# Kernel optimization log

Hardware: AMD Instinct MI355X
Metric: run time of the kernel (lower is better)

The kernel has to match this reference:

```python
import jax, jax.numpy as jnp
import numpy as np

S = 1.0   # scale s
M = 0.4   # margin m
EPS = 1e-12  # F.normalize eps


def _l2norm_rows(a):
    # F.normalize(a, dim=1): row-wise L2 normalization
    n = jnp.linalg.norm(a, axis=1, keepdims=True)
    return a / jnp.maximum(n, EPS)


def _half_loss(sim):
    # unique-label branch: positive is the diagonal, all off-diagonal are negatives
    N = sim.shape[0]
    num = S * (jnp.diagonal(sim) - M)                       # [N]
    offdiag = jnp.exp(S * sim) * (1.0 - jnp.eye(N, dtype=sim.dtype))
    denom = jnp.exp(num) + jnp.sum(offdiag, axis=1)         # [N]
    return num - jnp.log(denom)


def setup_inputs() -> dict:
    key = jax.random.key(0)
    k1, k2 = jax.random.split(key)
    N, D = 8192, 256
    return {
        "x1": jax.random.normal(k1, (N, D), dtype=jnp.float32),
        "x2": jax.random.normal(k2, (N, D), dtype=jnp.float32),
        "sentence_id": jnp.arange(N, dtype=jnp.int32),  # unique labels -> more_label=False branch
    }


def reference(x1, x2, sentence_id):
    # x12[i,j] row-normalized similarity of x1_i against all x2_j (and symmetric)
    x12 = _l2norm_rows(x1 @ x2.T)   # [N, N]
    x21 = _l2norm_rows(x2 @ x1.T)   # [N, N]
    L12 = _half_loss(x12)
    L21 = _half_loss(x21)
    loss = -jnp.mean(L12) - jnp.mean(L21)
    return loss, L12, L21
```

## Files before the change

### kernel.cpp

```cpp
#include <hip/hip_runtime.h>
#include <cstdint>
#include <cstddef>


#define NROWS 8192
#define DIMK 256
#define MARGIN 0.4f
#define LOG2E 1.4426950408889634f
#define LN2 0.6931471805599453f

typedef short short8 __attribute__((ext_vector_type(8)));
typedef float f32x4 __attribute__((ext_vector_type(4)));

__device__ __forceinline__ unsigned short f2bf(float f) {
  union { float f; unsigned u; } v; v.f = f;
  unsigned r = (v.u + 0x7fffu + ((v.u >> 16) & 1u)) >> 16;
  return (unsigned short)r;
}

__device__ __forceinline__ unsigned char f2fp8(float f) {
  union { float f; unsigned u; } v; v.f = f;
  const unsigned s = (v.u >> 24) & 0x80u;
  const unsigned au = v.u & 0x7fffffffu;
  if (au >= 0x43e00000u) return (unsigned char)(s | 0x7eu);
  int e = (int)(au >> 23) - 127;
  if (e >= -6) {
    unsigned mfull = (au & 0x7fffffu) | 0x800000u;
    unsigned r = (mfull + 0x7ffffu + ((mfull >> 20) & 1u)) >> 20;
    if (r == 16u) { r = 8u; ++e; }
    return (unsigned char)(s | ((unsigned)(e + 7) << 3) | (r & 7u));
  }
  float scaled = __builtin_fabsf(f) * 512.0f;
  unsigned n = (unsigned)(scaled + 0.5f);
  if (n >= 8u) return (unsigned char)(s | 0x08u);
  return (unsigned char)(s | n);
}

__device__ __forceinline__ void gl_lds16(const void* g, void* l) {
  __builtin_amdgcn_global_load_lds((const __attribute__((address_space(1))) void*)g,
                                   (__attribute__((address_space(3))) void*)l, 16, 0, 0);
}

__device__ __forceinline__ float fexp(float x) {
  return __builtin_amdgcn_exp2f(x * LOG2E);
}

__global__ __launch_bounds__(256)
void k_prep(const float* __restrict__ x1, const float* __restrict__ x2,
            unsigned short* __restrict__ Ab, unsigned short* __restrict__ Bb,
            unsigned char* __restrict__ A8, unsigned char* __restrict__ B8,
            float* __restrict__ diag, float* __restrict__ zero_region) {
  const int t = threadIdx.x;
  if (blockIdx.x < 2048) {
    const int row = blockIdx.x * 4 + (t >> 6);
    const int l = t & 63;
    const float4 a = ((const float4*)(x1 + (size_t)row * DIMK))[l];
    const float4 b = ((const float4*)(x2 + (size_t)row * DIMK))[l];
    ushort4 ua, ub;
    ua.x = f2bf(a.x); ua.y = f2bf(a.y); ua.z = f2bf(a.z); ua.w = f2bf(a.w);
    ub.x = f2bf(b.x); ub.y = f2bf(b.y); ub.z = f2bf(b.z); ub.w = f2bf(b.w);
    ((ushort4*)(Ab + (size_t)row * DIMK))[l] = ua;
    ((ushort4*)(Bb + (size_t)row * DIMK))[l] = ub;
    uchar4 qa, qb;
    qa.x = f2fp8(a.x); qa.y = f2fp8(a.y); qa.z = f2fp8(a.z); qa.w = f2fp8(a.w);
    qb.x = f2fp8(b.x); qb.y = f2fp8(b.y); qb.z = f2fp8(b.z); qb.w = f2fp8(b.w);
    ((uchar4*)(A8 + (size_t)row * DIMK))[l] = qa;
    ((uchar4*)(B8 + (size_t)row * DIMK))[l] = qb;
    float d = a.x * b.x + a.y * b.y + a.z * b.z + a.w * b.w;
#pragma unroll
    for (int m = 1; m < 64; m <<= 1) d += __shfl_xor(d, m);
    if (l == 0) diag[row] = d;
  } else {
    const size_t off = (size_t)(blockIdx.x - 2048) * 1024 + t * 4;
    float4 z = {0.f, 0.f, 0.f, 0.f};
    *(float4*)(zero_region + off) = z;
  }
}

__global__ __launch_bounds__(256)
void k_syrk(const unsigned short* __restrict__ Ab, const unsigned short* __restrict__ Bb,
            float* __restrict__ M1, float* __restrict__ M2) {
  __shared__ unsigned short As[64 * 32];
  __shared__ unsigned short Bs[64 * 32];
  const int t = threadIdx.x, w = t >> 6, l = t & 63, quad = l >> 4, l15 = l & 15;
  const int mat = blockIdx.z & 1;
  const int kseg = blockIdx.z >> 1;
  const unsigned short* X = mat ? Bb : Ab;
  float* Mo = mat ? M2 : M1;
  const int a0 = blockIdx.y * 64, b0 = blockIdx.x * 64;
  const int wr = (w >> 1) * 32, wc = (w & 1) * 32;
  f32x4 acc[2][2] = {};
  const int nn = t & 31, cb = t >> 5;
  const int c0 = cb * 8;
  const int nb = kseg * 512;
  for (int n0 = nb; n0 < nb + 512; n0 += 32) {
    short8 va = *(const short8*)(X + (size_t)(n0 + nn) * DIMK + a0 + c0);
    short8 vb = *(const short8*)(X + (size_t)(n0 + nn) * DIMK + b0 + c0);
#pragma unroll
    for (int i = 0; i < 8; ++i) {
      const int c = c0 + i;
      const int sl = (((nn >> 3) ^ ((c >> 1) & 3)) << 3) + (nn & 7);
      As[c * 32 + sl] = va[i];
      Bs[c * 32 + sl] = vb[i];
    }
    __syncthreads();
    short8 af[2], bg[2];
#pragma unroll
    for (int i = 0; i < 2; ++i) {
      const int ra = wr + i * 16 + l15;
      af[i] = *(const short8*)&As[ra * 32 + ((quad ^ ((ra >> 1) & 3)) << 3)];
      const int rb = wc + i * 16 + l15;
      bg[i] = *(const short8*)&Bs[rb * 32 + ((quad ^ ((rb >> 1) & 3)) << 3)];
    }
#pragma unroll
    for (int i = 0; i < 2; ++i)
#pragma unroll
      for (int j = 0; j < 2; ++j)
        acc[i][j] = __builtin_amdgcn_mfma_f32_16x16x32_bf16(af[i], bg[j], acc[i][j], 0, 0, 0);
    __syncthreads();
  }
#pragma unroll
  for (int i = 0; i < 2; ++i)
#pragma unroll
    for (int j = 0; j < 2; ++j)
#pragma unroll
      for (int r = 0; r < 4; ++r) {
        const int lr = wr + i * 16 + quad * 4 + r;
        const int lc = wc + j * 16 + l15;
        atomicAdd(&Mo[(size_t)(a0 + lr) * 256 + b0 + lc], acc[i][j][r]);
      }
}

__global__ __launch_bounds__(256)
void k_gemmN(const unsigned short* __restrict__ Ab, const unsigned short* __restrict__ Bb,
             const float* __restrict__ M1, const float* __restrict__ M2,
             const float* __restrict__ x1, const float* __restrict__ x2,
             float* __restrict__ rowsq, float* __restrict__ colsq) {
  __shared__ unsigned short As[2][4096];
  __shared__ unsigned short Bs[2][4096];
  const int t = threadIdx.x, w = t >> 6, l = t & 63, quad = l >> 4, l15 = l & 15;
  const unsigned short* A;
  const float* Mf;
  const float* Xf;
  float* sq;
  if (blockIdx.z == 0) { A = Ab; Mf = M2; Xf = x1; sq = rowsq; }
  else                 { A = Bb; Mf = M1; Xf = x2; sq = colsq; }
  const int row0 = blockIdx.x * 128;
  const int col0 = blockIdx.y * 128;
  const int wr = (w >> 1) * 64, wc = (w & 1) * 64;
  f32x4 acc[4][4] = {};

  const int sr0 = l >> 2, slot = l & 3;
  const int cA = w * 2, cB = w * 2 + 1;
  const int rA = cA * 16 + sr0, rB = cB * 16 + sr0;
  const int scA = (slot ^ ((rA >> 1) & 3)) << 3;
  const int scB = (slot ^ ((rB >> 1) & 3)) << 3;
  const unsigned short* pA0 = A + (size_t)(row0 + rA) * DIMK + scA;
  const unsigned short* pA1 = A + (size_t)(row0 + rB) * DIMK + scB;
  const int dA0 = cA * 512 + l * 8, dA1 = cB * 512 + l * 8;

  auto stageB = [&](int k0, int buf) {
#pragma unroll
    for (int g = 0; g < 2; ++g) {
      const int e = g * 2048 + t * 8;
      const int c = e >> 5, kk = e & 31;
      const float4 v0 = *(const float4*)(Mf + (size_t)(col0 + c) * 256 + k0 + kk);
      const float4 v1 = *(const float4*)(Mf + (size_t)(col0 + c) * 256 + k0 + kk + 4);
      ushort4 u0, u1;
      u0.x = f2bf(v0.x); u0.y = f2bf(v0.y); u0.z = f2bf(v0.z); u0.w = f2bf(v0.w);
      u1.x = f2bf(v1.x); u1.y = f2bf(v1.y); u1.z = f2bf(v1.z); u1.w = f2bf(v1.w);
      const int sw = ((kk >> 3) ^ ((c >> 1) & 3)) << 3;
      *(ushort4*)&Bs[buf][c * 32 + sw] = u0;
      *(ushort4*)&Bs[buf][c * 32 + sw + 4] = u1;
    }
  };
  auto issueA = [&](int k0, int buf) {
    gl_lds16(pA0 + k0, &As[buf][dA0]);
    gl_lds16(pA1 + k0, &As[buf][dA1]);
  };

  stageB(0, 0);
  issueA(0, 0);
#pragma unroll
  for (int k = 0; k < 8; ++k) {
    const int cur = k & 1;
    __syncthreads();
    if (k < 7) { stageB((k + 1) * 32, cur ^ 1); issueA((k + 1) * 32, cur ^ 1); }
    short8 af[4], bg[4];
#pragma unroll
    for (int i = 0; i < 4; ++i) {
      const int ra = wr + i * 16 + l15;
      af[i] = *(const short8*)&As[cur][ra * 32 + ((quad ^ ((ra >> 1) & 3)) << 3)];
      const int rb = wc + i * 16 + l15;
      bg[i] = *(const short8*)&Bs[cur][rb * 32 + ((quad ^ ((rb >> 1) & 3)) << 3)];
    }
#pragma unroll
    for (int i = 0; i < 4; ++i)
#pragma unroll
      for (int j = 0; j < 4; ++j)
        acc[i][j] = __builtin_amdgcn_mfma_f32_16x16x32_bf16(af[i], bg[j], acc[i][j], 0, 0, 0);
  }

#pragma unroll
  for (int i = 0; i < 4; ++i) {
#pragma unroll
    for (int r = 0; r < 4; ++r) {
      const int lr = wr + i * 16 + quad * 4 + r;
      const float* xr = Xf + (size_t)(row0 + lr) * DIMK + col0 + wc;
      float rp = 0.f;
#pragma unroll
      for (int j = 0; j < 4; ++j) rp += acc[i][j][r] * xr[j * 16 + l15];
      rp += __shfl_xor(rp, 1); rp += __shfl_xor(rp, 2);
      rp += __shfl_xor(rp, 4); rp += __shfl_xor(rp, 8);
      if (l15 == 0) atomicAdd(&sq[row0 + lr], rp);
    }
  }
}

__global__ __launch_bounds__(256)
void k_gemmE(const unsigned char* __restrict__ A8, const unsigned char* __restrict__ B8,
             const float* __restrict__ rowsq, const float* __restrict__ colsq,
             float* __restrict__ rowExp, float* __restrict__ colExp) {
  __shared__ unsigned char As[2][8192];
  __shared__ unsigned char Bs[2][8192];
  __shared__ float cRow[128];
  __shared__ float cCol[128];

  const int t = threadIdx.x;
  const int w = t >> 6;
  const int l = t & 63;
  const int quad = l >> 4;
  const int l15 = l & 15;
  const int row0 = blockIdx.x * 128;
  const int col0 = blockIdx.y * 128;
  const int wr = (w >> 1) * 64;
  const int wc = (w & 1) * 64;

  if (t < 128) cRow[t] = LOG2E * rsqrtf(rowsq[row0 + t]);
  else cCol[t - 128] = LOG2E * rsqrtf(colsq[col0 + t - 128]);

  f32x4 acc[4][4] = {};

  const int srow = t >> 1;
  const int shalf = (t & 1) * 16;
  const unsigned char* gA = A8 + (size_t)(row0 + srow) * DIMK + shalf;
  const unsigned char* gB = B8 + (size_t)(col0 + srow) * DIMK + shalf;
  const int d0 = t * 16, d1 = 4096 + t * 16;

  auto issue = [&](int k0, int buf) {
    gl_lds16(gA + k0, &As[buf][d0]);
    gl_lds16(gA + k0 + 32, &As[buf][d1]);
    gl_lds16(gB + k0, &Bs[buf][d0]);
    gl_lds16(gB + k0 + 32, &Bs[buf][d1]);
  };

  issue(0, 0);
#pragma unroll
  for (int it = 0; it < 4; ++it) {
    const int cur = it & 1;
    __syncthreads();
    if (it < 3) issue((it + 1) * 64, cur ^ 1);
#pragma unroll
    for (int kc = 0; kc < 2; ++kc) {
      long a_[4], b_[4];
#pragma unroll
      for (int i = 0; i < 4; ++i) {
        const int ra = wr + i * 16 + l15;
        a_[i] = *(const long*)&As[cur][kc * 4096 + ra * 32 + quad * 8];
        const int rb = wc + i * 16 + l15;
        b_[i] = *(const long*)&Bs[cur][kc * 4096 + rb * 32 + quad * 8];
      }
#pragma unroll
      for (int i = 0; i < 4; ++i)
#pragma unroll
        for (int j = 0; j < 4; ++j)
          acc[i][j] = __builtin_amdgcn_mfma_f32_16x16x32_fp8_fp8(a_[i], b_[j], acc[i][j], 0, 0, 0);
    }
  }

  float cj[4];
#pragma unroll
  for (int j = 0; j < 4; ++j) cj[j] = cCol[wc + j * 16 + l15];
  float colpart[4] = {0.f, 0.f, 0.f, 0.f};
#pragma unroll
  for (int i = 0; i < 4; ++i) {
#pragma unroll
    for (int r = 0; r < 4; ++r) {
      const int lr = wr + i * 16 + quad * 4 + r;
      const float ci = cRow[lr];
      float rp = 0.f;
#pragma unroll
      for (int j = 0; j < 4; ++j) {
        const float g = acc[i][j][r];
        rp += __builtin_amdgcn_exp2f(g * ci);
        colpart[j] += __builtin_amdgcn_exp2f(g * cj[j]);
      }
      rp += __shfl_xor(rp, 1); rp += __shfl_xor(rp, 2);
      rp += __shfl_xor(rp, 4); rp += __shfl_xor(rp, 8);
      if (l15 == 0) atomicAdd(&rowExp[row0 + lr], rp);
    }
  }
#pragma unroll
  for (int j = 0; j < 4; ++j) {
    float cp = colpart[j];
    cp += __shfl_xor(cp, 16); cp += __shfl_xor(cp, 32);
    if (l < 16) atomicAdd(&colExp[col0 + wc + j * 16 + l15], cp);
  }
}

__global__ __launch_bounds__(1024)
void k_final(const float* __restrict__ rowsq, const float* __restrict__ colsq,
             const float* __restrict__ diag, const float* __restrict__ rowExp,
             const float* __restrict__ colExp, float* __restrict__ out,
             double* __restrict__ lossAcc, int* __restrict__ doneCnt) {
  const int t = threadIdx.x;
  const int i = blockIdx.x * 1024 + t;
  const float d = diag[i];
  const float s1 = d * rsqrtf(rowsq[i]);
  const float s2 = d * rsqrtf(colsq[i]);
  const float n1 = s1 - MARGIN, n2 = s2 - MARGIN;
  const float L1 = n1 - LN2 * __builtin_amdgcn_logf(rowExp[i] - fexp(s1) + fexp(n1));
  const float L2 = n2 - LN2 * __builtin_amdgcn_logf(colExp[i] - fexp(s2) + fexp(n2));
  out[1 + i] = L1;
  out[1 + NROWS + i] = L2;
  double part = (double)L1 + (double)L2;
#pragma unroll
  for (int m = 1; m < 64; m <<= 1) part += __shfl_xor(part, m);
  __shared__ double red[16];
  if ((t & 63) == 0) red[t >> 6] = part;
  __syncthreads();
  if (t == 0) {
    double s = 0.0;
#pragma unroll
    for (int q = 0; q < 16; ++q) s += red[q];
    atomicAdd(lossAcc, s);
    __threadfence();
    if (atomicAdd(doneCnt, 1) == 7) {
      const double la =
          __hip_atomic_load(lossAcc, __ATOMIC_ACQUIRE, __HIP_MEMORY_SCOPE_AGENT);
      out[0] = (float)(-la / (double)NROWS);
    }
  }
}

extern "C" void kernel_launch(void* const* d_in, const int* in_sizes, int n_in,
                              void* d_out, int out_size, void* d_ws, size_t ws_size,
                              hipStream_t stream) {
  const float* x1 = (const float*)d_in[0];
  const float* x2 = (const float*)d_in[1];
  float* out = (float*)d_out;
  char* ws = (char*)d_ws;

  unsigned short* Ab = (unsigned short*)(ws);
  unsigned short* Bb = (unsigned short*)(ws + 4194304);
  float* M1 = (float*)(ws + 8388608);
  float* M2 = (float*)(ws + 8650752);
  float* rowsq = (float*)(ws + 8912896);
  float* colsq = (float*)(ws + 8945664);
  float* rowExp = (float*)(ws + 8978432);
  float* colExp = (float*)(ws + 9011200);
  char* ctrl = ws + 9043968;
  double* lossAcc = (double*)(ctrl);
  int* doneCnt = (int*)(ctrl + 256);
  float* diag = (float*)(ws + 9048064);
  unsigned char* A8 = (unsigned char*)(ws + 9080832);
  unsigned char* B8 = (unsigned char*)(ws + 11177984);

  k_prep<<<2209, 256, 0, stream>>>(x1, x2, Ab, Bb, A8, B8, diag,
                                   (float*)(ws + 8388608));
  k_syrk<<<dim3(4, 4, 32), 256, 0, stream>>>(Ab, Bb, M1, M2);
  k_gemmN<<<dim3(64, 2, 2), 256, 0, stream>>>(Ab, Bb, M1, M2, x1, x2, rowsq, colsq);
  k_gemmE<<<dim3(64, 64), 256, 0, stream>>>(A8, B8, rowsq, colsq, rowExp, colExp);
  k_final<<<8, 1024, 0, stream>>>(rowsq, colsq, diag, rowExp, colExp, out,
                                  lossAcc, doneCnt);
}
```

Measured before the change: 188.7 us.

## Double-buffer syrk staging and stream fp32 Gram tiles directly into LDS

k_syrk now double-buffers its LDS tiles, with one barrier per step, and writes packed 32-bit pairs instead of scalar shorts. Each block covers twice the K range, so the launch halves the split-K count and the number of atomic adds. k_gemmN stops converting the M matrices to bf16 in registers before storing to LDS. It loads fp32 directly with async global-to-LDS copies and converts to bf16 when building fragments, at the cost of double the LDS footprint and simpler rounding.

Result: slower. 197.8 us (+4.8%).

```diff
diff --git a/kernel.cpp b/kernel.cpp
--- a/kernel.cpp
+++ b/kernel.cpp
@@ -80,8 +80,8 @@
 __global__ __launch_bounds__(256)
 void k_syrk(const unsigned short* __restrict__ Ab, const unsigned short* __restrict__ Bb,
             float* __restrict__ M1, float* __restrict__ M2) {
-  __shared__ unsigned short As[64 * 32];
-  __shared__ unsigned short Bs[64 * 32];
+  __shared__ unsigned short As[2][2048];
+  __shared__ unsigned short Bs[2][2048];
   const int t = threadIdx.x, w = t >> 6, l = t & 63, quad = l >> 4, l15 = l & 15;
   const int mat = blockIdx.z & 1;
   const int kseg = blockIdx.z >> 1;
@@ -90,34 +90,48 @@
   const int a0 = blockIdx.y * 64, b0 = blockIdx.x * 64;
   const int wr = (w >> 1) * 32, wc = (w & 1) * 32;
   f32x4 acc[2][2] = {};
-  const int nn = t & 31, cb = t >> 5;
-  const int c0 = cb * 8;
-  const int nb = kseg * 512;
-  for (int n0 = nb; n0 < nb + 512; n0 += 32) {
-    short8 va = *(const short8*)(X + (size_t)(n0 + nn) * DIMK + a0 + c0);
-    short8 vb = *(const short8*)(X + (size_t)(n0 + nn) * DIMK + b0 + c0);
-#pragma unroll
-    for (int i = 0; i < 8; ++i) {
+  const int n2 = t & 15, c0 = (t >> 4) * 4;
+  const int nb = kseg * 1024;
+
+  auto stage = [&](int n0, int buf) {
+    const unsigned short* r0 = X + (size_t)(n0 + 2 * n2) * DIMK;
+    const unsigned short* r1 = X + (size_t)(n0 + 2 * n2 + 1) * DIMK;
+    const ushort4 a0v = *(const ushort4*)(r0 + a0 + c0);
+    const ushort4 a1v = *(const ushort4*)(r1 + a0 + c0);
+    const ushort4 b0v = *(const ushort4*)(r0 + b0 + c0);
+    const ushort4 b1v = *(const ushort4*)(r1 + b0 + c0);
+    const unsigned short pa0[4] = {a0v.x, a0v.y, a0v.z, a0v.w};
+    const unsigned short pa1[4] = {a1v.x, a1v.y, a1v.z, a1v.w};
+    const unsigned short pb0[4] = {b0v.x, b0v.y, b0v.z, b0v.w};
+    const unsigned short pb1[4] = {b1v.x, b1v.y, b1v.z, b1v.w};
+#pragma unroll
+    for (int i = 0; i < 4; ++i) {
       const int c = c0 + i;
-      const int sl = (((nn >> 3) ^ ((c >> 1) & 3)) << 3) + (nn & 7);
-      As[c * 32 + sl] = va[i];
-      Bs[c * 32 + sl] = vb[i];
-    }
+      const int ss = (n2 >> 2) ^ ((c >> 1) & 3);
+      const int pos = c * 32 + ss * 8 + ((2 * n2) & 7);
+      *(unsigned*)&As[buf][pos] = (unsigned)pa0[i] | ((unsigned)pa1[i] << 16);
+      *(unsigned*)&Bs[buf][pos] = (unsigned)pb0[i] | ((unsigned)pb1[i] << 16);
+    }
+  };
+
+  stage(nb, 0);
+  for (int it = 0; it < 32; ++it) {
+    const int cur = it & 1;
     __syncthreads();
+    if (it < 31) stage(nb + (it + 1) * 32, cur ^ 1);
     short8 af[2], bg[2];
 #pragma unroll
     for (int i = 0; i < 2; ++i) {
       const int ra = wr + i * 16 + l15;
-      af[i] = *(const short8*)&As[ra * 32 + ((quad ^ ((ra >> 1) & 3)) << 3)];
+      af[i] = *(const short8*)&As[cur][ra * 32 + ((quad ^ ((ra >> 1) & 3)) << 3)];
       const int rb = wc + i * 16 + l15;
-      bg[i] = *(const short8*)&Bs[rb * 32 + ((quad ^ ((rb >> 1) & 3)) << 3)];
+      bg[i] = *(const short8*)&Bs[cur][rb * 32 + ((quad ^ ((rb >> 1) & 3)) << 3)];
     }
 #pragma unroll
     for (int i = 0; i < 2; ++i)
 #pragma unroll
       for (int j = 0; j < 2; ++j)
         acc[i][j] = __builtin_amdgcn_mfma_f32_16x16x32_bf16(af[i], bg[j], acc[i][j], 0, 0, 0);
-    __syncthreads();
   }
 #pragma unroll
   for (int i = 0; i < 2; ++i)
@@ -137,7 +151,7 @@
              const float* __restrict__ x1, const float* __restrict__ x2,
              float* __restrict__ rowsq, float* __restrict__ colsq) {
   __shared__ unsigned short As[2][4096];
-  __shared__ unsigned short Bs[2][4096];
+  __shared__ float Bsf[2][4096];
   const int t = threadIdx.x, w = t >> 6, l = t & 63, quad = l >> 4, l15 = l & 15;
   const unsigned short* A;
   const float* Mf;
@@ -159,40 +173,45 @@
   const unsigned short* pA1 = A + (size_t)(row0 + rB) * DIMK + scB;
   const int dA0 = cA * 512 + l * 8, dA1 = cB * 512 + l * 8;
 
-  auto stageB = [&](int k0, int buf) {
-#pragma unroll
-    for (int g = 0; g < 2; ++g) {
-      const int e = g * 2048 + t * 8;
-      const int c = e >> 5, kk = e & 31;
-      const float4 v0 = *(const float4*)(Mf + (size_t)(col0 + c) * 256 + k0 + kk);
-      const float4 v1 = *(const float4*)(Mf + (size_t)(col0 + c) * 256 + k0 + kk + 4);
-      ushort4 u0, u1;
-      u0.x = f2bf(v0.x); u0.y = f2bf(v0.y); u0.z = f2bf(v0.z); u0.w = f2bf(v0.w);
-      u1.x = f2bf(v1.x); u1.y = f2bf(v1.y); u1.z = f2bf(v1.z); u1.w = f2bf(v1.w);
-      const int sw = ((kk >> 3) ^ ((c >> 1) & 3)) << 3;
-      *(ushort4*)&Bs[buf][c * 32 + sw] = u0;
-      *(ushort4*)&Bs[buf][c * 32 + sw + 4] = u1;
-    }
-  };
-  auto issueA = [&](int k0, int buf) {
+  const int brow = t >> 3, bslot = t & 7;
+  auto issue = [&](int k0, int buf) {
     gl_lds16(pA0 + k0, &As[buf][dA0]);
     gl_lds16(pA1 + k0, &As[buf][dA1]);
+#pragma unroll
+    for (int p = 0; p < 4; ++p) {
+      const int row = p * 32 + brow;
+      const int ss = bslot ^ (row & 7);
+      gl_lds16(Mf + (size_t)(col0 + row) * 256 + k0 + ss * 4,
+               &Bsf[buf][p * 1024 + t * 4]);
+    }
   };
 
-  stageB(0, 0);
-  issueA(0, 0);
+  auto bfrag = [&](int buf, int rb) -> short8 {
+    const int m = rb & 7;
+    const f32x4 lo = *(const f32x4*)&Bsf[buf][rb * 32 + (((2 * quad) ^ m) << 2)];
+    const f32x4 hi = *(const f32x4*)&Bsf[buf][rb * 32 + (((2 * quad + 1) ^ m) << 2)];
+    short8 r;
+#pragma unroll
+    for (int e = 0; e < 4; ++e) {
+      union { float f; unsigned u; } v;
+      v.f = lo[e]; r[e] = (short)((v.u + 0x8000u) >> 16);
+      v.f = hi[e]; r[4 + e] = (short)((v.u + 0x8000u) >> 16);
+    }
+    return r;
+  };
+
+  issue(0, 0);
 #pragma unroll
   for (int k = 0; k < 8; ++k) {
     const int cur = k & 1;
     __syncthreads();
-    if (k < 7) { stageB((k + 1) * 32, cur ^ 1); issueA((k + 1) * 32, cur ^ 1); }
+    if (k < 7) issue((k + 1) * 32, cur ^ 1);
     short8 af[4], bg[4];
 #pragma unroll
     for (int i = 0; i < 4; ++i) {
       const int ra = wr + i * 16 + l15;
       af[i] = *(const short8*)&As[cur][ra * 32 + ((quad ^ ((ra >> 1) & 3)) << 3)];
-      const int rb = wc + i * 16 + l15;
-      bg[i] = *(const short8*)&Bs[cur][rb * 32 + ((quad ^ ((rb >> 1) & 3)) << 3)];
+      bg[i] = bfrag(cur, wc + i * 16 + l15);
     }
 #pragma unroll
     for (int i = 0; i < 4; ++i)
@@ -368,7 +387,7 @@
 
   k_prep<<<2209, 256, 0, stream>>>(x1, x2, Ab, Bb, A8, B8, diag,
                                    (float*)(ws + 8388608));
-  k_syrk<<<dim3(4, 4, 32), 256, 0, stream>>>(Ab, Bb, M1, M2);
+  k_syrk<<<dim3(4, 4, 16), 256, 0, stream>>>(Ab, Bb, M1, M2);
   k_gemmN<<<dim3(64, 2, 2), 256, 0, stream>>>(Ab, Bb, M1, M2, x1, x2, rowsq, colsq);
   k_gemmE<<<dim3(64, 64), 256, 0, stream>>>(A8, B8, rowsq, colsq, rowExp, colExp);
   k_final<<<8, 1024, 0, stream>>>(rowsq, colsq, diag, rowExp, colExp, out,
```
